# Kernel tuning notes

Measured on AMD Instinct MI355X. Metric: run time of the kernel, lower is better.

Reference implementation:

```python
import jax, jax.numpy as jnp
import numpy as np

N = 50000      # nodes
E = 500000     # edges
G = 8          # graphs in batch
H = 64         # latent width (message_passer out_channels)
FIN = 5        # raw node feature dim
MDIM = 3       # mask dim (last col = BC flag)
EF = 3         # edge feature dim
OUT = 4        # output dim
REPEATS = 4    # message passing repeats


def _mlp(h, w1, b1, w2, b2):
    return jnp.dot(jax.nn.relu(jnp.dot(h, w1) + b1), w2) + b2


def _seg_mean(v, idx, n):
    s = jax.ops.segment_sum(v, idx, num_segments=n)
    c = jax.ops.segment_sum(jnp.ones((v.shape[0], 1), v.dtype), idx, num_segments=n)
    return s / jnp.maximum(c, 1.0)


def _lin(k, fi, fo):
    return (jax.random.normal(k, (fi, fo), jnp.float32) / np.sqrt(fi),
            jnp.zeros((fo,), jnp.float32))


def setup_inputs() -> dict:
    key = jax.random.key(0)
    ks = jax.random.split(key, 16)
    x = jax.random.normal(ks[0], (N, FIN), jnp.float32)
    x_mask = jax.random.uniform(ks[1], (N, MDIM), jnp.float32)
    x_mask = x_mask.at[:, -1].set((x_mask[:, -1] > 0.9).astype(jnp.float32))
    edge_index = jax.random.randint(ks[2], (2, E), 0, N, jnp.int32)
    edge_attr = jax.random.normal(ks[3], (E, EF), jnp.float32)
    pos = jax.random.uniform(ks[4], (N, 2), jnp.float32)
    batch = jnp.sort(jax.random.randint(ks[5], (N,), 0, G, jnp.int32))
    enc_w1, enc_b1 = _lin(ks[6], FIN + MDIM, H)
    enc_w2, enc_b2 = _lin(ks[7], H, H)
    msg_w1, msg_b1 = _lin(ks[8], 2 * H + EF, H)
    msg_w2, msg_b2 = _lin(ks[9], H, H)
    upd_w1, upd_b1 = _lin(ks[10], 4 * H, H)
    upd_w2, upd_b2 = _lin(ks[11], H, H)
    dec_w1, dec_b1 = _lin(ks[12], H, H)
    dec_w2, dec_b2 = _lin(ks[13], H, OUT)
    return dict(x=x, x_mask=x_mask, edge_index=edge_index, edge_attr=edge_attr,
                pos=pos, batch=batch,
                enc_w1=enc_w1, enc_b1=enc_b1, enc_w2=enc_w2, enc_b2=enc_b2,
                msg_w1=msg_w1, msg_b1=msg_b1, msg_w2=msg_w2, msg_b2=msg_b2,
                upd_w1=upd_w1, upd_b1=upd_b1, upd_w2=upd_w2, upd_b2=upd_b2,
                dec_w1=dec_w1, dec_b1=dec_b1, dec_w2=dec_w2, dec_b2=dec_b2)


def reference(x, x_mask, edge_index, edge_attr, pos, batch,
              enc_w1, enc_b1, enc_w2, enc_b2,
              msg_w1, msg_b1, msg_w2, msg_b2,
              upd_w1, upd_b1, upd_w2, upd_b2,
              dec_w1, dec_b1, dec_w2, dec_b2):
    # x = concat([x, x_mask]); BC_idxs = x_mask[:, -1]
    bc = x_mask[:, -1:]                                   # [N,1] 0/1 BC flag
    h = _mlp(jnp.concatenate([x, x_mask], axis=1), enc_w1, enc_b1, enc_w2, enc_b2)
    # x_BC = scatter-mean of encoded BC nodes per graph (mask-weighted segment mean)
    bc_sum = jax.ops.segment_sum(h * bc, batch, num_segments=G)
    bc_cnt = jax.ops.segment_sum(bc, batch, num_segments=G)
    x_BC = bc_sum / jnp.maximum(bc_cnt, 1.0)              # [G,H]
    x_graph = _seg_mean(h, batch, G)                      # global_mean_pool [G,H]
    src, dst = edge_index[0], edge_index[1]
    for _ in range(REPEATS):
        # message: MLP over [x_src, x_dst, edge_attr], scatter-mean to dst
        m = _mlp(jnp.concatenate([h[src], h[dst], edge_attr], axis=1),
                 msg_w1, msg_b1, msg_w2, msg_b2)          # [E,H]
        agg = _seg_mean(m, dst, N)                        # [N,H]
        # node update conditioned on global and BC context, residual
        h = h + _mlp(jnp.concatenate([h, agg, x_graph[batch], x_BC[batch]], axis=1),
                     upd_w1, upd_b1, upd_w2, upd_b2)
        x_graph = _seg_mean(h, batch, G)                  # refreshed each repeat
    return _mlp(h, dec_w1, dec_b1, dec_w2, dec_b2)        # [N,OUT]
```

## Files before the change

kernel.cpp:

```cpp
#include <hip/hip_runtime.h>
#include <hip/hip_bf16.h>

#define NN 50000
#define EE 500000
#define GG 8
#define NB 196

#define SCALE_A 65536.0f
#define INV_SCALE_A (1.0f/65536.0f)
#define SCALE_G 16777216.0f
#define INV_SCALE_G (1.0f/16777216.0f)

using short8 = __attribute__((ext_vector_type(8))) short;
using f32x16 = __attribute__((ext_vector_type(16))) float;

__device__ __forceinline__ float4 ld4(const float* p){ return *reinterpret_cast<const float4*>(p); }

__device__ __forceinline__ short f2b(float f){
  union { __hip_bfloat16 b; short s; } u;
  u.b = __float2bfloat16(f);
  return u.s;
}

__global__ __launch_bounds__(256) void k_count(const int* __restrict__ dst, int* __restrict__ cnt){
  int e = blockIdx.x*256 + threadIdx.x;
  if (e < EE) atomicAdd(&cnt[dst[e]], 1);
}

__global__ __launch_bounds__(256) void k_scanA(const int* __restrict__ cnt, int* __restrict__ bsum){
  __shared__ int s[256];
  int t = threadIdx.x;
  int i = blockIdx.x*256 + t;
  s[t] = (i < NN) ? cnt[i] : 0;
  __syncthreads();
  for (int o=128;o>0;o>>=1){ if (t<o) s[t]+=s[t+o]; __syncthreads(); }
  if (t==0) bsum[blockIdx.x] = s[0];
}

__global__ __launch_bounds__(256) void k_scanB(const int* __restrict__ bsum, int* __restrict__ boff){
  __shared__ int s[256];
  int t = threadIdx.x;
  s[t] = (t < NB) ? bsum[t] : 0;
  __syncthreads();
  for (int o=1;o<256;o<<=1){
    int u = (t>=o) ? s[t-o] : 0;
    __syncthreads();
    s[t] += u;
    __syncthreads();
  }
  if (t < NB) boff[t] = (t==0) ? 0 : s[t-1];
}

__global__ __launch_bounds__(256) void k_scanC_prep(const int* __restrict__ cnt, const int* __restrict__ boff,
                                               int* __restrict__ offs,
                                               float* __restrict__ inv, const int* __restrict__ batch,
                                               const float* __restrict__ xm,
                                               float* __restrict__ ncnt, float* __restrict__ bccnt){
  __shared__ int s[256];
  __shared__ float lc[GG], lb[GG];
  int t = threadIdx.x;
  int i = blockIdx.x*256 + t;
  if (t < GG){ lc[t]=0.f; lb[t]=0.f; }
  int v = (i < NN) ? cnt[i] : 0;
  s[t] = v;
  __syncthreads();
  for (int o=1;o<256;o<<=1){
    int u = (t>=o) ? s[t-o] : 0;
    __syncthreads();
    s[t] += u;
    __syncthreads();
  }
  if (i < NN){
    offs[i] = boff[blockIdx.x] + s[t] - v;
    inv[i] = 1.0f / fmaxf((float)v, 1.0f);
    int g = batch[i];
    atomicAdd(&lc[g], 1.0f);
    atomicAdd(&lb[g], xm[i*3+2]);
  }
  __syncthreads();
  if (t < GG){ atomicAdd(&ncnt[t], lc[t]); atomicAdd(&bccnt[t], lb[t]); }
}

__global__ __launch_bounds__(256) void k_prep(const int* __restrict__ cnt, float* __restrict__ inv,
                       const int* __restrict__ batch, const float* __restrict__ xm,
                       float* __restrict__ ncnt, float* __restrict__ bccnt){
  __shared__ float lc[GG], lb[GG];
  int t = threadIdx.x;
  if (t < GG){ lc[t]=0.f; lb[t]=0.f; }
  __syncthreads();
  int i = blockIdx.x*256 + t;
  if (i < NN){
    inv[i] = 1.0f / fmaxf((float)cnt[i], 1.0f);
    int g = batch[i];
    atomicAdd(&lc[g], 1.0f);
    atomicAdd(&lb[g], xm[i*3+2]);
  }
  __syncthreads();
  if (t < GG){ atomicAdd(&ncnt[t], lc[t]); atomicAdd(&bccnt[t], lb[t]); }
}

__global__ __launch_bounds__(256) void k_scat1(const int* __restrict__ dst, int* __restrict__ offs,
                                               int* __restrict__ perm){
  int e = blockIdx.x*256 + threadIdx.x;
  if (e >= EE) return;
  int d = dst[e];
  int pos = atomicAdd(&offs[d], 1);
  perm[pos] = e;
}

__global__ __launch_bounds__(256) void k_scat2(const int* __restrict__ perm,
                                               const int* __restrict__ src, const int* __restrict__ dst,
                                               const float* __restrict__ ea,
                                               int* __restrict__ srcs_s, int* __restrict__ dsts_s,
                                               short* __restrict__ ea16){
  int i = blockIdx.x*256 + threadIdx.x;
  if (i >= EE) return;
  int e = perm[i];
  srcs_s[i] = src[e];
  dsts_s[i] = dst[e];
  int lo = ((int)(unsigned short)f2b(ea[(size_t)e*3+0])) |
           (((int)(unsigned short)f2b(ea[(size_t)e*3+1])) << 16);
  int hi = ((int)(unsigned short)f2b(ea[(size_t)e*3+2]));
  int2 v; v.x = lo; v.y = hi;
  *(int2*)(ea16 + (size_t)i*4) = v;
}

__device__ __forceinline__ void packone(const float* __restrict__ w, int Kreal, int idx, short* __restrict__ out){
  int k = idx >> 6, n = idx & 63;
  float v = (k < Kreal) ? w[k*64 + n] : 0.f;
  int ks = k >> 4, kl = k & 15;
  int lane = (n & 31) + 32*(kl >> 3);
  int e = kl & 7;
  out[(ks*2 + (n>>5))*512 + lane*8 + e] = f2b(v);
}

__global__ __launch_bounds__(256) void k_wpack(
    const float* __restrict__ mw1, const float* __restrict__ mw2,
    const float* __restrict__ uw1, const float* __restrict__ uw2,
    short* __restrict__ mw1p, short* __restrict__ mw2p,
    short* __restrict__ uw1p, short* __restrict__ uw2p){
  int gid = blockIdx.x*256 + threadIdx.x;
  int stride = gridDim.x*256;
  for (int i=gid; i<144*64; i+=stride) packone(mw1, 131, i, mw1p);
  for (int i=gid; i<64*64;  i+=stride) packone(mw2, 64,  i, mw2p);
  for (int i=gid; i<256*64; i+=stride) packone(uw1, 256, i, uw1p);
  for (int i=gid; i<64*64;  i+=stride) packone(uw2, 64,  i, uw2p);
}

__global__ __launch_bounds__(256) void k_enc(
    const float* __restrict__ x, const float* __restrict__ xm,
    const float* __restrict__ w1, const float* __restrict__ b1,
    const float* __restrict__ w2, const float* __restrict__ b2,
    float* __restrict__ h, short* __restrict__ h16){
  __shared__ float w1s[8*64];
  __shared__ float w2s[64*64];
  __shared__ float b1s[64], b2s[64];
  __shared__ float ols[4][64][17];
  int t = threadIdx.x;
  for (int i=t;i<8*64;i+=256) w1s[i]=w1[i];
  for (int i=t;i<64*64;i+=256) w2s[i]=w2[i];
  if (t<64){ b1s[t]=b1[t]; b2s[t]=b2[t]; }
  __syncthreads();
  const int w = t >> 6, lane = t & 63;
  const int base_w = blockIdx.x*256 + w*64;
  const int n = base_w + lane;
  const int nc = (n < NN) ? n : (NN-1);
  float in[8];
  #pragma unroll
  for (int k=0;k<5;k++) in[k] = x[nc*5+k];
  #pragma unroll
  for (int k=0;k<3;k++) in[5+k] = xm[nc*3+k];
  float hid[64];
  #pragma unroll
  for (int o=0;o<64;o++){
    float a = b1s[o];
    #pragma unroll
    for (int k=0;k<8;k++) a += in[k]*w1s[k*64+o];
    hid[o] = fmaxf(a, 0.f);
  }
  for (int c=0;c<4;c++){
    float a[16];
    #pragma unroll
    for (int j=0;j<16;j++) a[j] = b2s[c*16+j];
    for (int k=0;k<64;k++){
      float hv = hid[k];
      #pragma unroll
      for (int j=0;j<16;j++) a[j] += hv * w2s[k*64 + c*16 + j];
    }
    #pragma unroll
    for (int j=0;j<16;j++) ols[w][lane][j] = a[j];
    __syncthreads();
    #pragma unroll
    for (int p=0;p<4;p++){
      int nd = p*16 + (lane>>2);
      int jj = lane & 3;
      int ng = base_w + nd;
      if (ng < NN){
        float4 v = make_float4(ols[w][nd][jj*4+0], ols[w][nd][jj*4+1],
                               ols[w][nd][jj*4+2], ols[w][nd][jj*4+3]);
        *(float4*)(h + (size_t)ng*64 + c*16 + jj*4) = v;
      }
    }
    #pragma unroll
    for (int p=0;p<2;p++){
      int nd = p*32 + (lane>>1);
      int jj = (lane & 1)*8;
      int ng = base_w + nd;
      if (ng < NN){
        short8 s;
        #pragma unroll
        for (int q=0;q<8;q++) s[q] = f2b(ols[w][nd][jj+q]);
        *(short8*)(h16 + (size_t)ng*64 + c*16 + jj) = s;
      }
    }
    __syncthreads();
  }
}

__global__ __launch_bounds__(256) void k_gred(
    const float* __restrict__ h, const int* __restrict__ batch,
    const float* __restrict__ xm,
    unsigned long long* __restrict__ xg_sum, unsigned long long* __restrict__ xbc_sum, int withBC){
  __shared__ float ls[4][GG][64];
  __shared__ float lb[4][GG][64];
  int t = threadIdx.x;
  int d = t & 63, grp = t >> 6;
  for (int g=0; g<GG; g++){ ls[grp][g][d]=0.f; lb[grp][g][d]=0.f; }
  __syncthreads();
  for (int i = blockIdx.x*4 + grp; i < NN; i += gridDim.x*4){
    int g = batch[i];
    float v = h[(size_t)i*64 + d];
    ls[grp][g][d] += v;
    if (withBC) lb[grp][g][d] += v * xm[i*3+2];
  }
  __syncthreads();
  if (t < 64){
    for (int g=0; g<GG; g++){
      float s = ls[0][g][d]+ls[1][g][d]+ls[2][g][d]+ls[3][g][d];
      atomicAdd(&xg_sum[g*64+d], (unsigned long long)(long long)llrintf(s*SCALE_G));
    }
  } else if (withBC && t < 128){
    int dd = t & 63;
    for (int g=0; g<GG; g++){
      float s = lb[0][g][dd]+lb[1][g][dd]+lb[2][g][dd]+lb[3][g][dd];
      atomicAdd(&xbc_sum[g*64+dd], (unsigned long long)(long long)llrintf(s*SCALE_G));
    }
  }
}

__global__ void k_gfin(unsigned long long* __restrict__ xg_sum, const unsigned long long* __restrict__ xbc_sum,
                       const float* __restrict__ ncnt, const float* __restrict__ bccnt,
                       short* __restrict__ xg16, short* __restrict__ xbc16, int withBC){
  int t = threadIdx.x;
  int g = t >> 6;
  float sg = (float)(long long)xg_sum[t] * INV_SCALE_G;
  xg16[t] = f2b(sg / fmaxf(ncnt[g], 1.f));
  xg_sum[t] = 0;
  if (withBC){
    float sb = (float)(long long)xbc_sum[t] * INV_SCALE_G;
    xbc16[t] = f2b(sb / fmaxf(bccnt[g], 1.f));
  }
}

__global__ __launch_bounds__(64) void k_msg_s(
    const short* __restrict__ h16,
    const int* __restrict__ srcs_s, const int* __restrict__ dsts_s,
    const short* __restrict__ ea16,
    const short* __restrict__ w1p, const float* __restrict__ b1,
    const short* __restrict__ w2p, const float* __restrict__ b2,
    int* __restrict__ agg,
    unsigned long long* __restrict__ xg_sum, const unsigned long long* __restrict__ xbc_sum,
    const float* __restrict__ ncnt, const float* __restrict__ bccnt,
    short* __restrict__ xg16, short* __restrict__ xbc16, int withBC){
  __shared__ int buf[2304];
  const int t = threadIdx.x;
  if (blockIdx.x == 0){
    for (int i=t; i<GG*64; i+=64){
      int g = i >> 6;
      float sg = (float)(long long)xg_sum[i] * INV_SCALE_G;
      xg16[i] = f2b(sg / fmaxf(ncnt[g], 1.f));
      xg_sum[i] = 0;
      if (withBC){
        float sb = (float)(long long)xbc_sum[i] * INV_SCALE_G;
        xbc16[i] = f2b(sb / fmaxf(bccnt[g], 1.f));
      }
    }
  }
  const int nwg = gridDim.x;
  const int q = nwg >> 3, rm = nwg & 7;
  const int xcd = blockIdx.x & 7, idx = blockIdx.x >> 3;
  const int wg = (xcd < rm ? xcd*(q+1) : rm*(q+1) + (xcd-rm)*q) + idx;
  const int base = wg * 64;

  const int lane = t;
  const int r = lane & 31, khalf = lane >> 5;
  const int slot = base + lane;
  const int dl = (slot < EE) ? dsts_s[slot] : -1;

  const int eA = base + r, eB = base + 32 + r;
  const bool vA = eA < EE, vB = eB < EE;
  const int sA = vA ? srcs_s[eA] : 0;
  const int sB = vB ? srcs_s[eB] : 0;
  int dA = __shfl(dl, r);        if (dA < 0) dA = 0;
  int dB = __shfl(dl, 32 + r);   if (dB < 0) dB = 0;

  float b1v0 = b1[r], b1v1 = b1[32 + r];
  f32x16 acc00, acc01, acc10, acc11;
  #pragma unroll
  for (int j=0;j<16;j++){ acc00[j]=b1v0; acc01[j]=b1v1; acc10[j]=b1v0; acc11[j]=b1v1; }

  const short8* w1f = (const short8*)w1p;
  #pragma unroll
  for (int ks=0; ks<9; ks++){
    short8 a0, a1;
    if (ks < 8){
      long offA, offB;
      if (ks < 4){
        offA = (long)sA*64 + ks*16 + khalf*8;
        offB = (long)sB*64 + ks*16 + khalf*8;
      } else {
        offA = (long)dA*64 + (ks-4)*16 + khalf*8;
        offB = (long)dB*64 + (ks-4)*16 + khalf*8;
      }
      a0 = *(const short8*)(h16 + offA);
      a1 = *(const short8*)(h16 + offB);
    } else {
      #pragma unroll
      for (int j=0;j<8;j++){ a0[j]=0; a1[j]=0; }
      if (khalf == 0){
        if (vA){
          int2 v = *(const int2*)(ea16 + (size_t)eA*4);
          a0[0]=(short)v.x; a0[1]=(short)(v.x>>16); a0[2]=(short)v.y; a0[3]=(short)(v.y>>16);
        }
        if (vB){
          int2 v = *(const int2*)(ea16 + (size_t)eB*4);
          a1[0]=(short)v.x; a1[1]=(short)(v.x>>16); a1[2]=(short)v.y; a1[3]=(short)(v.y>>16);
        }
      }
    }
    short8 bf0 = w1f[(ks*2+0)*64 + lane];
    short8 bf1 = w1f[(ks*2+1)*64 + lane];
    acc00 = __builtin_amdgcn_mfma_f32_32x32x16_bf16(a0, bf0, acc00, 0, 0, 0);
    acc01 = __builtin_amdgcn_mfma_f32_32x32x16_bf16(a0, bf1, acc01, 0, 0, 0);
    acc10 = __builtin_amdgcn_mfma_f32_32x32x16_bf16(a1, bf0, acc10, 0, 0, 0);
    acc11 = __builtin_amdgcn_mfma_f32_32x32x16_bf16(a1, bf1, acc11, 0, 0, 0);
  }

  short* hw = (short*)&buf[0];
  #pragma unroll
  for (int reg=0; reg<16; reg++){
    int row = (reg&3) + 8*(reg>>2) + 4*khalf;
    hw[(row     )*72 + r     ] = f2b(fmaxf(acc00[reg], 0.f));
    hw[(row     )*72 + 32 + r] = f2b(fmaxf(acc01[reg], 0.f));
    hw[(row + 32)*72 + r     ] = f2b(fmaxf(acc10[reg], 0.f));
    hw[(row + 32)*72 + 32 + r] = f2b(fmaxf(acc11[reg], 0.f));
  }

  float b2v0 = b2[r], b2v1 = b2[32 + r];
  f32x16 c00, c01, c10, c11;
  #pragma unroll
  for (int j=0;j<16;j++){ c00[j]=b2v0; c01[j]=b2v1; c10[j]=b2v0; c11[j]=b2v1; }

  const short8* w2f = (const short8*)w2p;
  #pragma unroll
  for (int ks=0; ks<4; ks++){
    short8 p0 = *(const short8*)(hw + (r     )*72 + ks*16 + khalf*8);
    short8 p1 = *(const short8*)(hw + (32 + r)*72 + ks*16 + khalf*8);
    short8 bf0 = w2f[(ks*2+0)*64 + lane];
    short8 bf1 = w2f[(ks*2+1)*64 + lane];
    c00 = __builtin_amdgcn_mfma_f32_32x32x16_bf16(p0, bf0, c00, 0, 0, 0);
    c01 = __builtin_amdgcn_mfma_f32_32x32x16_bf16(p0, bf1, c01, 0, 0, 0);
    c10 = __builtin_amdgcn_mfma_f32_32x32x16_bf16(p1, bf0, c10, 0, 0, 0);
    c11 = __builtin_amdgcn_mfma_f32_32x32x16_bf16(p1, bf1, c11, 0, 0, 0);
  }

  int* mb = &buf[0];

  #pragma unroll
  for (int reg=0; reg<16; reg++){
    int row = (reg&3) + 8*(reg>>2) + 4*khalf;
    mb[row*65 + r     ] = __float2int_rn(c00[reg]*SCALE_A);
    mb[row*65 + 32 + r] = __float2int_rn(c01[reg]*SCALE_A);
  }
  {
    int run = 0;
    #pragma unroll
    for (int rr=0; rr<32; rr++){ run += mb[rr*65 + lane]; mb[rr*65 + lane] = run; }
    int cur = 0;
    while (cur < 32){
      int d = __shfl(dl, cur);
      unsigned long long diff = __ballot(dl != d);
      unsigned low = (unsigned)diff;
      unsigned rest = low & (0xFFFFFFFEu << cur);
      int end = rest ? (__ffs(rest) - 1) : 32;
      if (d >= 0){
        int s = mb[(end-1)*65 + lane] - (cur ? mb[(cur-1)*65 + lane] : 0);
        atomicAdd(&agg[(size_t)d*64 + lane], s);
      }
      cur = end;
    }
  }

  #pragma unroll
  for (int reg=0; reg<16; reg++){
    int row = (reg&3) + 8*(reg>>2) + 4*khalf;
    mb[row*65 + r     ] = __float2int_rn(c10[reg]*SCALE_A);
    mb[row*65 + 32 + r] = __float2int_rn(c11[reg]*SCALE_A);
  }
  {
    int run = 0;
    #pragma unroll
    for (int rr=0; rr<32; rr++){ run += mb[rr*65 + lane]; mb[rr*65 + lane] = run; }
    int cur = 0;
    while (cur < 32){
      int d = __shfl(dl, 32 + cur);
      unsigned long long diff = __ballot(dl != d);
      unsigned hi = (unsigned)(diff >> 32);
      unsigned rest = hi & (0xFFFFFFFEu << cur);
      int end = rest ? (__ffs(rest) - 1) : 32;
      if (d >= 0){
        int s = mb[(end-1)*65 + lane] - (cur ? mb[(cur-1)*65 + lane] : 0);
        atomicAdd(&agg[(size_t)d*64 + lane], s);
      }
      cur = end;
    }
  }
}

__global__ __launch_bounds__(256) void k_msg_atomic(
    const short* __restrict__ h16, const int* __restrict__ src, const int* __restrict__ dst,
    const float* __restrict__ ea,
    const short* __restrict__ w1p, const float* __restrict__ b1,
    const short* __restrict__ w2p, const float* __restrict__ b2,
    int* __restrict__ agg){
  __shared__ short hidT[4][64*72];
  const int t = threadIdx.x;
  const int w = t >> 6, lane = t & 63;
  const int r = lane & 31, khalf = lane >> 5;
  const int base = blockIdx.x*256 + w*64;
  const int eA = base + r, eB = base + 32 + r;
  const bool vA = eA < EE, vB = eB < EE;
  const int sA = vA ? src[eA] : 0, dA_ = vA ? dst[eA] : 0;
  const int sB = vB ? src[eB] : 0, dB_ = vB ? dst[eB] : 0;

  float b1v0 = b1[r], b1v1 = b1[32 + r];
  f32x16 acc00, acc01, acc10, acc11;
  #pragma unroll
  for (int j=0;j<16;j++){ acc00[j]=b1v0; acc01[j]=b1v1; acc10[j]=b1v0; acc11[j]=b1v1; }

  const short8* w1f = (const short8*)w1p;
  #pragma unroll
  for (int ks=0; ks<9; ks++){
    short8 a0, a1;
    if (ks < 8){
      long offA, offB;
      if (ks < 4){
        offA = (long)sA*64 + ks*16 + khalf*8;
        offB = (long)sB*64 + ks*16 + khalf*8;
      } else {
        offA = (long)dA_*64 + (ks-4)*16 + khalf*8;
        offB = (long)dB_*64 + (ks-4)*16 + khalf*8;
      }
      a0 = *(const short8*)(h16 + offA);
      a1 = *(const short8*)(h16 + offB);
    } else {
      #pragma unroll
      for (int j=0;j<8;j++){ a0[j]=0; a1[j]=0; }
      if (khalf == 0){
        if (vA){ a0[0]=f2b(ea[3*eA]); a0[1]=f2b(ea[3*eA+1]); a0[2]=f2b(ea[3*eA+2]); }
        if (vB){ a1[0]=f2b(ea[3*eB]); a1[1]=f2b(ea[3*eB+1]); a1[2]=f2b(ea[3*eB+2]); }
      }
    }
    short8 bf0 = w1f[(ks*2+0)*64 + lane];
    short8 bf1 = w1f[(ks*2+1)*64 + lane];
    acc00 = __builtin_amdgcn_mfma_f32_32x32x16_bf16(a0, bf0, acc00, 0, 0, 0);
    acc01 = __builtin_amdgcn_mfma_f32_32x32x16_bf16(a0, bf1, acc01, 0, 0, 0);
    acc10 = __builtin_amdgcn_mfma_f32_32x32x16_bf16(a1, bf0, acc10, 0, 0, 0);
    acc11 = __builtin_amdgcn_mfma_f32_32x32x16_bf16(a1, bf1, acc11, 0, 0, 0);
  }

  short* hw = &hidT[w][0];
  #pragma unroll
  for (int reg=0; reg<16; reg++){
    int row = (reg&3) + 8*(reg>>2) + 4*khalf;
    hw[(row     )*72 + r     ] = f2b(fmaxf(acc00[reg], 0.f));
    hw[(row     )*72 + 32 + r] = f2b(fmaxf(acc01[reg], 0.f));
    hw[(row + 32)*72 + r     ] = f2b(fmaxf(acc10[reg], 0.f));
    hw[(row + 32)*72 + 32 + r] = f2b(fmaxf(acc11[reg], 0.f));
  }

  float b2v0 = b2[r], b2v1 = b2[32 + r];
  f32x16 c00, c01, c10, c11;
  #pragma unroll
  for (int j=0;j<16;j++){ c00[j]=b2v0; c01[j]=b2v1; c10[j]=b2v0; c11[j]=b2v1; }

  const short8* w2f = (const short8*)w2p;
  #pragma unroll
  for (int ks=0; ks<4; ks++){
    short8 a0 = *(const short8*)(hw + (r     )*72 + ks*16 + khalf*8);
    short8 a1 = *(const short8*)(hw + (32 + r)*72 + ks*16 + khalf*8);
    short8 bf0 = w2f[(ks*2+0)*64 + lane];
    short8 bf1 = w2f[(ks*2+1)*64 + lane];
    c00 = __builtin_amdgcn_mfma_f32_32x32x16_bf16(a0, bf0, c00, 0, 0, 0);
    c01 = __builtin_amdgcn_mfma_f32_32x32x16_bf16(a0, bf1, c01, 0, 0, 0);
    c10 = __builtin_amdgcn_mfma_f32_32x32x16_bf16(a1, bf0, c10, 0, 0, 0);
    c11 = __builtin_amdgcn_mfma_f32_32x32x16_bf16(a1, bf1, c11, 0, 0, 0);
  }

  #pragma unroll
  for (int reg=0; reg<16; reg++){
    int row = (reg&3) + 8*(reg>>2) + 4*khalf;
    int e0r = base + row;
    int e1r = base + 32 + row;
    int d0 = __shfl(dA_, row);
    int d1 = __shfl(dB_, row);
    if (e0r < EE){
      atomicAdd(&agg[(size_t)d0*64 + r     ], __float2int_rn(c00[reg]*SCALE_A));
      atomicAdd(&agg[(size_t)d0*64 + 32 + r], __float2int_rn(c01[reg]*SCALE_A));
    }
    if (e1r < EE){
      atomicAdd(&agg[(size_t)d1*64 + r     ], __float2int_rn(c10[reg]*SCALE_A));
      atomicAdd(&agg[(size_t)d1*64 + 32 + r], __float2int_rn(c11[reg]*SCALE_A));
    }
  }
}

__global__ __launch_bounds__(64) void k_upd(
    float* __restrict__ h32, short* __restrict__ h16,
    int* __restrict__ agg, const float* __restrict__ inv,
    const int* __restrict__ batch,
    const short* __restrict__ xg16, const short* __restrict__ xbc16,
    const short* __restrict__ w1p, const float* __restrict__ b1,
    const short* __restrict__ w2p, const float* __restrict__ b2,
    unsigned long long* __restrict__ xg_sum, int withG){
  __shared__ short hidT[32*72];
  __shared__ unsigned long long gs[GG*64];
  const int t = threadIdx.x;
  for (int i=t; i<GG*64; i+=64) gs[i]=0;
  __syncthreads();

  const int lane = t;
  const int r = lane & 31, khalf = lane >> 5;
  const int n0 = blockIdx.x*32;
  const int n = n0 + r;
  const int nc = (n < NN) ? n : (NN-1);
  const int g = batch[nc];
  const float sc = inv[nc] * INV_SCALE_A;

  float b1v0 = b1[r], b1v1 = b1[32 + r];
  f32x16 a0acc, a1acc;
  #pragma unroll
  for (int j=0;j<16;j++){ a0acc[j]=b1v0; a1acc[j]=b1v1; }

  const short8* w1f = (const short8*)w1p;
  #pragma unroll
  for (int ks=0; ks<16; ks++){
    short8 a;
    int so = (ks & 3)*16 + khalf*8;
    if (ks < 4){
      a = *(const short8*)(h16 + (long)nc*64 + so);
    } else if (ks < 8){
      int4 i0 = *(const int4*)(agg + (long)nc*64 + so);
      int4 i1 = *(const int4*)(agg + (long)nc*64 + so + 4);
      if (n < NN){
        *(int4*)(agg + (long)nc*64 + so)     = make_int4(0,0,0,0);
        *(int4*)(agg + (long)nc*64 + so + 4) = make_int4(0,0,0,0);
      }
      a[0]=f2b((float)i0.x*sc); a[1]=f2b((float)i0.y*sc); a[2]=f2b((float)i0.z*sc); a[3]=f2b((float)i0.w*sc);
      a[4]=f2b((float)i1.x*sc); a[5]=f2b((float)i1.y*sc); a[6]=f2b((float)i1.z*sc); a[7]=f2b((float)i1.w*sc);
    } else if (ks < 12){
      a = *(const short8*)(xg16 + g*64 + so);
    } else {
      a = *(const short8*)(xbc16 + g*64 + so);
    }
    short8 bf0 = w1f[(ks*2+0)*64 + lane];
    short8 bf1 = w1f[(ks*2+1)*64 + lane];
    a0acc = __builtin_amdgcn_mfma_f32_32x32x16_bf16(a, bf0, a0acc, 0, 0, 0);
    a1acc = __builtin_amdgcn_mfma_f32_32x32x16_bf16(a, bf1, a1acc, 0, 0, 0);
  }

  short* hw = hidT;
  #pragma unroll
  for (int reg=0; reg<16; reg++){
    int row = (reg&3) + 8*(reg>>2) + 4*khalf;
    hw[row*72 + r     ] = f2b(fmaxf(a0acc[reg], 0.f));
    hw[row*72 + 32 + r] = f2b(fmaxf(a1acc[reg], 0.f));
  }

  float b2v0 = b2[r], b2v1 = b2[32 + r];
  f32x16 c0, c1;
  #pragma unroll
  for (int j=0;j<16;j++){ c0[j]=b2v0; c1[j]=b2v1; }

  const short8* w2f = (const short8*)w2p;
  #pragma unroll
  for (int ks=0; ks<4; ks++){
    short8 a = *(const short8*)(hw + r*72 + ks*16 + khalf*8);
    short8 bf0 = w2f[(ks*2+0)*64 + lane];
    short8 bf1 = w2f[(ks*2+1)*64 + lane];
    c0 = __builtin_amdgcn_mfma_f32_32x32x16_bf16(a, bf0, c0, 0, 0, 0);
    c1 = __builtin_amdgcn_mfma_f32_32x32x16_bf16(a, bf1, c1, 0, 0, 0);
  }

  const bool doG = (withG != 0);
  const int g0 = __shfl(g, 0), g31 = __shfl(g, 31);
  const bool uni = (g0 == g31);
  long long s0 = 0, s1 = 0;
  #pragma unroll
  for (int reg=0; reg<16; reg++){
    int row = (reg&3) + 8*(reg>>2) + 4*khalf;
    int gg = __shfl(g, row);
    int nn = n0 + row;
    if (nn < NN){
      size_t i0 = (size_t)nn*64 + r;
      float v0 = h32[i0] + c0[reg];
      float v1 = h32[i0+32] + c1[reg];
      h32[i0] = v0;    h16[i0] = f2b(v0);
      h32[i0+32] = v1; h16[i0+32] = f2b(v1);
      if (doG){
        long long q0 = llrintf(v0*SCALE_G), q1 = llrintf(v1*SCALE_G);
        if (uni){ s0 += q0; s1 += q1; }
        else {
          atomicAdd(&gs[gg*64 + r     ], (unsigned long long)q0);
          atomicAdd(&gs[gg*64 + 32 + r], (unsigned long long)q1);
        }
      }
    }
  }
  if (doG && uni && (s0|s1)){
    atomicAdd(&gs[g0*64 + r     ], (unsigned long long)s0);
    atomicAdd(&gs[g0*64 + 32 + r], (unsigned long long)s1);
  }
  __syncthreads();
  if (doG){
    for (int i=t; i<GG*64; i+=64){
      unsigned long long v = gs[i];
      if (v) atomicAdd(&xg_sum[i], v);
    }
  }
}

__global__ __launch_bounds__(256) void k_dec(
    const float* __restrict__ h,
    const float* __restrict__ w1, const float* __restrict__ b1,
    const float* __restrict__ w2, const float* __restrict__ b2,
    float* __restrict__ out){
  __shared__ float w1s[64*64];
  __shared__ float w2s[64*4];
  __shared__ float b1s[64], b2s[4];
  int t=threadIdx.x;
  for (int i=t;i<64*64;i+=256) w1s[i]=w1[i];
  for (int i=t;i<256;i+=256) w2s[i]=w2[i];
  if (t<64) b1s[t]=b1[t];
  if (t<4) b2s[t]=b2[t];
  __syncthreads();
  int n = blockIdx.x*256+t;
  if (n>=NN) return;
  float xr[64];
  #pragma unroll
  for (int k=0;k<16;k++){
    float4 v = ld4(h + (size_t)n*64 + k*4);
    xr[k*4+0]=v.x; xr[k*4+1]=v.y; xr[k*4+2]=v.z; xr[k*4+3]=v.w;
  }
  float a0=b2s[0],a1=b2s[1],a2=b2s[2],a3=b2s[3];
  for (int o=0;o<64;o++){
    float a=b1s[o];
    #pragma unroll
    for (int k=0;k<64;k++) a += xr[k]*w1s[k*64+o];
    a = fmaxf(a,0.f);
    a0 += a*w2s[o*4+0]; a1 += a*w2s[o*4+1]; a2 += a*w2s[o*4+2]; a3 += a*w2s[o*4+3];
  }
  out[(size_t)n*4+0]=a0; out[(size_t)n*4+1]=a1; out[(size_t)n*4+2]=a2; out[(size_t)n*4+3]=a3;
}

extern "C" void kernel_launch(void* const* d_in, const int* in_sizes, int n_in,
                              void* d_out, int out_size, void* d_ws, size_t ws_size,
                              hipStream_t stream){
  const float* x   = (const float*)d_in[0];
  const float* xm  = (const float*)d_in[1];
  const int*   ei  = (const int*)d_in[2];
  const float* ea  = (const float*)d_in[3];
  const int* batch = (const int*)d_in[5];
  const float* enc_w1=(const float*)d_in[6],  *enc_b1=(const float*)d_in[7];
  const float* enc_w2=(const float*)d_in[8],  *enc_b2=(const float*)d_in[9];
  const float* msg_w1=(const float*)d_in[10], *msg_b1=(const float*)d_in[11];
  const float* msg_w2=(const float*)d_in[12], *msg_b2=(const float*)d_in[13];
  const float* upd_w1=(const float*)d_in[14], *upd_b1=(const float*)d_in[15];
  const float* upd_w2=(const float*)d_in[16], *upd_b2=(const float*)d_in[17];
  const float* dec_w1=(const float*)d_in[18], *dec_b1=(const float*)d_in[19];
  const float* dec_w2=(const float*)d_in[20], *dec_b2=(const float*)d_in[21];
  const int* srcp = ei;
  const int* dstp = ei + EE;

  char* ws = (char*)d_ws;
  float* h32     = (float*)(ws + 0);
  int*   agg     = (int*)  (ws + 12800000);
  int*   cnt     = (int*)  (ws + 25600000);
  unsigned long long* xg_sum  = (unsigned long long*)(ws + 25800000);
  unsigned long long* xbc_sum = (unsigned long long*)(ws + 25804096);
  float* ncnt    = (float*)(ws + 25808192);
  float* bccnt   = (float*)(ws + 25808224);
  short* h16     = (short*)(ws + 25808256);
  float* inv     = (float*)(ws + 32208256);
  short* xg16    = (short*)(ws + 32408256);
  short* xbc16   = (short*)(ws + 32409280);
  short* mw1p    = (short*)(ws + 32410304);
  short* mw2p    = (short*)(ws + 32428736);
  short* uw1p    = (short*)(ws + 32436928);
  short* uw2p    = (short*)(ws + 32469696);
  int*   offs    = (int*)  (ws + 32477888);
  int*   srcs_s  = (int*)  (ws + 32677888);
  int*   dsts_s  = (int*)  (ws + 34678784);
  short* ea16s   = (short*)(ws + 36679680);
  int*   bsum    = (int*)  (ws + 40681472);
  int*   boff    = (int*)  (ws + 40682272);
  int*   perm    = (int*)  (ws + 40683072);
  const size_t WS_NEED_SORT = 42683968;
  const int useSort = (ws_size >= WS_NEED_SORT) ? 1 : 0;

  hipMemsetAsync(ws + 12800000, 0, 13008256, stream);
  k_wpack<<<34, 256, 0, stream>>>(msg_w1, msg_w2, upd_w1, upd_w2, mw1p, mw2p, uw1p, uw2p);
  k_count<<<(EE+255)/256, 256, 0, stream>>>(dstp, cnt);
  if (useSort){
    k_scanA<<<NB, 256, 0, stream>>>(cnt, bsum);
    k_scanB<<<1, 256, 0, stream>>>(bsum, boff);
    k_scanC_prep<<<NB, 256, 0, stream>>>(cnt, boff, offs, inv, batch, xm, ncnt, bccnt);
    k_scat1<<<(EE+255)/256, 256, 0, stream>>>(dstp, offs, perm);
    k_scat2<<<(EE+255)/256, 256, 0, stream>>>(perm, srcp, dstp, ea, srcs_s, dsts_s, ea16s);
  } else {
    k_prep<<<(NN+255)/256, 256, 0, stream>>>(cnt, inv, batch, xm, ncnt, bccnt);
  }
  k_enc<<<(NN+255)/256, 256, 0, stream>>>(x, xm, enc_w1, enc_b1, enc_w2, enc_b2, h32, h16);
  k_gred<<<512, 256, 0, stream>>>(h32, batch, xm, xg_sum, xbc_sum, 1);

  if (useSort){
    for (int rp=0; rp<4; rp++){
      k_msg_s<<<(EE+63)/64, 64, 0, stream>>>(h16, srcs_s, dsts_s, ea16s, mw1p, msg_b1, mw2p, msg_b2, agg,
                                             xg_sum, xbc_sum, ncnt, bccnt, xg16, xbc16, (rp==0)?1:0);
      int withG = (rp < 3) ? 1 : 0;
      k_upd<<<(NN+31)/32, 64, 0, stream>>>(h32, h16, agg, inv, batch, xg16, xbc16, uw1p, upd_b1, uw2p, upd_b2, xg_sum, withG);
    }
  } else {
    k_gfin<<<1, 512, 0, stream>>>(xg_sum, xbc_sum, ncnt, bccnt, xg16, xbc16, 1);
    for (int rp=0; rp<4; rp++){
      k_msg_atomic<<<(EE+255)/256, 256, 0, stream>>>(h16, srcp, dstp, ea, mw1p, msg_b1, mw2p, msg_b2, agg);
      int withG = (rp < 3) ? 1 : 0;
      k_upd<<<(NN+31)/32, 64, 0, stream>>>(h32, h16, agg, inv, batch, xg16, xbc16, uw1p, upd_b1, uw2p, upd_b2, xg_sum, withG);
      if (withG) k_gfin<<<1, 512, 0, stream>>>(xg_sum, xbc_sum, ncnt, bccnt, xg16, xbc16, 0);
    }
  }
  k_dec<<<(NN+255)/256, 256, 0, stream>>>(h32, dec_w1, dec_b1, dec_w2, dec_b2, (float*)d_out);
}
```

Before: 399.8 us.

## Fuse message pass and node update into per-node-block round kernel

Replaces the separate edge-parallel message kernel and node update kernel with one kernel per round. Each workgroup owns 32 destination nodes, walks their dst-sorted edge range, accumulates messages in LDS instead of global atomics, and then runs the update MLP in the same workgroup. h16 is double-buffered so neighbour reads in a round see the previous h, and graph-mean sums go to per-round buffers. This removes the agg round trip through global memory, the global atomics and the memset, at the cost of load imbalance from uneven node degrees and a grid that is about ten times smaller.

```diff
diff --git a/kernel.cpp b/kernel.cpp
--- a/kernel.cpp
+++ b/kernel.cpp
@@ -262,167 +262,256 @@
   }
 }
 
-__global__ __launch_bounds__(64) void k_msg_s(
-    const short* __restrict__ h16,
+__global__ __launch_bounds__(64) void k_round(
+    const short* __restrict__ h16in, short* __restrict__ h16out,
+    float* __restrict__ h32,
     const int* __restrict__ srcs_s, const int* __restrict__ dsts_s,
     const short* __restrict__ ea16,
-    const short* __restrict__ w1p, const float* __restrict__ b1,
-    const short* __restrict__ w2p, const float* __restrict__ b2,
-    int* __restrict__ agg,
-    unsigned long long* __restrict__ xg_sum, const unsigned long long* __restrict__ xbc_sum,
+    const int* __restrict__ offsEnd, const int* __restrict__ cnt,
+    const float* __restrict__ inv, const int* __restrict__ batch,
+    const unsigned long long* __restrict__ xgs_prev,
+    unsigned long long* __restrict__ xgs_next,
+    const unsigned long long* __restrict__ xbc_sum,
     const float* __restrict__ ncnt, const float* __restrict__ bccnt,
-    short* __restrict__ xg16, short* __restrict__ xbc16, int withBC){
+    const short* __restrict__ mw1p, const float* __restrict__ mb1,
+    const short* __restrict__ mw2p, const float* __restrict__ mb2,
+    const short* __restrict__ uw1p, const float* __restrict__ ub1,
+    const short* __restrict__ uw2p, const float* __restrict__ ub2,
+    int withG){
+  __shared__ int nodeagg[32*65];
   __shared__ int buf[2304];
+  __shared__ short xgloc[GG*64];
+  __shared__ short xbcloc[GG*64];
   const int t = threadIdx.x;
-  if (blockIdx.x == 0){
-    for (int i=t; i<GG*64; i+=64){
-      int g = i >> 6;
-      float sg = (float)(long long)xg_sum[i] * INV_SCALE_G;
-      xg16[i] = f2b(sg / fmaxf(ncnt[g], 1.f));
-      xg_sum[i] = 0;
-      if (withBC){
-        float sb = (float)(long long)xbc_sum[i] * INV_SCALE_G;
-        xbc16[i] = f2b(sb / fmaxf(bccnt[g], 1.f));
-      }
-    }
-  }
-  const int nwg = gridDim.x;
-  const int q = nwg >> 3, rm = nwg & 7;
-  const int xcd = blockIdx.x & 7, idx = blockIdx.x >> 3;
-  const int wg = (xcd < rm ? xcd*(q+1) : rm*(q+1) + (xcd-rm)*q) + idx;
-  const int base = wg * 64;
-
-  const int lane = t;
-  const int r = lane & 31, khalf = lane >> 5;
-  const int slot = base + lane;
-  const int dl = (slot < EE) ? dsts_s[slot] : -1;
-
-  const int eA = base + r, eB = base + 32 + r;
-  const bool vA = eA < EE, vB = eB < EE;
-  const int sA = vA ? srcs_s[eA] : 0;
-  const int sB = vB ? srcs_s[eB] : 0;
-  int dA = __shfl(dl, r);        if (dA < 0) dA = 0;
-  int dB = __shfl(dl, 32 + r);   if (dB < 0) dB = 0;
-
-  float b1v0 = b1[r], b1v1 = b1[32 + r];
-  f32x16 acc00, acc01, acc10, acc11;
-  #pragma unroll
-  for (int j=0;j<16;j++){ acc00[j]=b1v0; acc01[j]=b1v1; acc10[j]=b1v0; acc11[j]=b1v1; }
-
-  const short8* w1f = (const short8*)w1p;
-  #pragma unroll
-  for (int ks=0; ks<9; ks++){
-    short8 a0, a1;
-    if (ks < 8){
-      long offA, offB;
-      if (ks < 4){
-        offA = (long)sA*64 + ks*16 + khalf*8;
-        offB = (long)sB*64 + ks*16 + khalf*8;
+  const int lane = t, r = lane & 31, khalf = lane >> 5;
+
+  for (int i=t; i<GG*64; i+=64){
+    int g = i >> 6;
+    xgloc[i]  = f2b((float)(long long)xgs_prev[i] * INV_SCALE_G / fmaxf(ncnt[g], 1.f));
+    xbcloc[i] = f2b((float)(long long)xbc_sum[i] * INV_SCALE_G / fmaxf(bccnt[g], 1.f));
+  }
+  for (int i=t; i<32*65; i+=64) nodeagg[i] = 0;
+
+  const int n0 = blockIdx.x * 32;
+  const int nLast = ((n0 + 32 <= NN) ? (n0 + 32) : NN) - 1;
+  const int eStart = offsEnd[n0] - cnt[n0];
+  const int eEnd   = offsEnd[nLast];
+
+  const float b1v0 = mb1[r], b1v1 = mb1[32 + r];
+  const float b2v0 = mb2[r], b2v1 = mb2[32 + r];
+  const short8* w1f = (const short8*)mw1p;
+  const short8* w2f = (const short8*)mw2p;
+  short* hw = (short*)&buf[0];
+  int* mb = &buf[0];
+
+  for (int ebase = eStart; ebase < eEnd; ebase += 64){
+    const int slot = ebase + lane;
+    const int dl = (slot < eEnd) ? (dsts_s[slot] - n0) : -1;
+    const int slotA = ebase + r, slotB = ebase + 32 + r;
+    const bool vA = slotA < eEnd, vB = slotB < eEnd;
+    const int sA = vA ? srcs_s[slotA] : 0;
+    const int sB = vB ? srcs_s[slotB] : 0;
+    int dAl = __shfl(dl, r);      const int dA = n0 + (dAl < 0 ? 0 : dAl);
+    int dBl = __shfl(dl, 32 + r); const int dB = n0 + (dBl < 0 ? 0 : dBl);
+
+    f32x16 acc00, acc01, acc10, acc11;
+    #pragma unroll
+    for (int j=0;j<16;j++){ acc00[j]=b1v0; acc01[j]=b1v1; acc10[j]=b1v0; acc11[j]=b1v1; }
+
+    #pragma unroll
+    for (int ks=0; ks<9; ks++){
+      short8 a0, a1;
+      if (ks < 8){
+        long offA = (ks < 4) ? ((long)sA*64 + ks*16 + khalf*8) : ((long)dA*64 + (ks-4)*16 + khalf*8);
+        long offB = (ks < 4) ? ((long)sB*64 + ks*16 + khalf*8) : ((long)dB*64 + (ks-4)*16 + khalf*8);
+        a0 = *(const short8*)(h16in + offA);
+        a1 = *(const short8*)(h16in + offB);
       } else {
-        offA = (long)dA*64 + (ks-4)*16 + khalf*8;
-        offB = (long)dB*64 + (ks-4)*16 + khalf*8;
-      }
-      a0 = *(const short8*)(h16 + offA);
-      a1 = *(const short8*)(h16 + offB);
+        #pragma unroll
+        for (int j=0;j<8;j++){ a0[j]=0; a1[j]=0; }
+        if (khalf == 0){
+          if (vA){
+            int2 v = *(const int2*)(ea16 + (size_t)slotA*4);
+            a0[0]=(short)v.x; a0[1]=(short)(v.x>>16); a0[2]=(short)v.y; a0[3]=(short)(v.y>>16);
+          }
+          if (vB){
+            int2 v = *(const int2*)(ea16 + (size_t)slotB*4);
+            a1[0]=(short)v.x; a1[1]=(short)(v.x>>16); a1[2]=(short)v.y; a1[3]=(short)(v.y>>16);
+          }
+        }
+      }
+      short8 bf0 = w1f[(ks*2+0)*64 + lane];
+      short8 bf1 = w1f[(ks*2+1)*64 + lane];
+      acc00 = __builtin_amdgcn_mfma_f32_32x32x16_bf16(a0, bf0, acc00, 0, 0, 0);
+      acc01 = __builtin_amdgcn_mfma_f32_32x32x16_bf16(a0, bf1, acc01, 0, 0, 0);
+      acc10 = __builtin_amdgcn_mfma_f32_32x32x16_bf16(a1, bf0, acc10, 0, 0, 0);
+      acc11 = __builtin_amdgcn_mfma_f32_32x32x16_bf16(a1, bf1, acc11, 0, 0, 0);
+    }
+
+    #pragma unroll
+    for (int reg=0; reg<16; reg++){
+      int row = (reg&3) + 8*(reg>>2) + 4*khalf;
+      hw[(row     )*72 + r     ] = f2b(fmaxf(acc00[reg], 0.f));
+      hw[(row     )*72 + 32 + r] = f2b(fmaxf(acc01[reg], 0.f));
+      hw[(row + 32)*72 + r     ] = f2b(fmaxf(acc10[reg], 0.f));
+      hw[(row + 32)*72 + 32 + r] = f2b(fmaxf(acc11[reg], 0.f));
+    }
+
+    f32x16 c00, c01, c10, c11;
+    #pragma unroll
+    for (int j=0;j<16;j++){ c00[j]=b2v0; c01[j]=b2v1; c10[j]=b2v0; c11[j]=b2v1; }
+
+    #pragma unroll
+    for (int ks=0; ks<4; ks++){
+      short8 p0 = *(const short8*)(hw + (r     )*72 + ks*16 + khalf*8);
+      short8 p1 = *(const short8*)(hw + (32 + r)*72 + ks*16 + khalf*8);
+      short8 bf0 = w2f[(ks*2+0)*64 + lane];
+      short8 bf1 = w2f[(ks*2+1)*64 + lane];
+      c00 = __builtin_amdgcn_mfma_f32_32x32x16_bf16(p0, bf0, c00, 0, 0, 0);
+      c01 = __builtin_amdgcn_mfma_f32_32x32x16_bf16(p0, bf1, c01, 0, 0, 0);
+      c10 = __builtin_amdgcn_mfma_f32_32x32x16_bf16(p1, bf0, c10, 0, 0, 0);
+      c11 = __builtin_amdgcn_mfma_f32_32x32x16_bf16(p1, bf1, c11, 0, 0, 0);
+    }
+
+    #pragma unroll
+    for (int reg=0; reg<16; reg++){
+      int row = (reg&3) + 8*(reg>>2) + 4*khalf;
+      mb[row*65 + r     ] = __float2int_rn(c00[reg]*SCALE_A);
+      mb[row*65 + 32 + r] = __float2int_rn(c01[reg]*SCALE_A);
+    }
+    {
+      int run = 0;
+      #pragma unroll
+      for (int rr=0; rr<32; rr++){ run += mb[rr*65 + lane]; mb[rr*65 + lane] = run; }
+      int cur = 0;
+      while (cur < 32){
+        int d = __shfl(dl, cur);
+        unsigned long long diff = __ballot(dl != d);
+        unsigned low = (unsigned)diff;
+        unsigned rest = low & (0xFFFFFFFEu << cur);
+        int end = rest ? (__ffs(rest) - 1) : 32;
+        if (d >= 0){
+          int s = mb[(end-1)*65 + lane] - (cur ? mb[(cur-1)*65 + lane] : 0);
+          nodeagg[d*65 + lane] += s;
+        }
+        cur = end;
+      }
+    }
+
+    #pragma unroll
+    for (int reg=0; reg<16; reg++){
+      int row = (reg&3) + 8*(reg>>2) + 4*khalf;
+      mb[row*65 + r     ] = __float2int_rn(c10[reg]*SCALE_A);
+      mb[row*65 + 32 + r] = __float2int_rn(c11[reg]*SCALE_A);
+    }
+    {
+      int run = 0;
+      #pragma unroll
+      for (int rr=0; rr<32; rr++){ run += mb[rr*65 + lane]; mb[rr*65 + lane] = run; }
+      int cur = 0;
+      while (cur < 32){
+        int d = __shfl(dl, 32 + cur);
+        unsigned long long diff = __ballot(dl != d);
+        unsigned hi = (unsigned)(diff >> 32);
+        unsigned rest = hi & (0xFFFFFFFEu << cur);
+        int end = rest ? (__ffs(rest) - 1) : 32;
+        if (d >= 0){
+          int s = mb[(end-1)*65 + lane] - (cur ? mb[(cur-1)*65 + lane] : 0);
+          nodeagg[d*65 + lane] += s;
+        }
+        cur = end;
+      }
+    }
+  }
+
+  const int n = n0 + r;
+  const int nc = (n < NN) ? n : (NN-1);
+  const int g = batch[nc];
+  const float sc = inv[nc] * INV_SCALE_A;
+
+  float ub1v0 = ub1[r], ub1v1 = ub1[32 + r];
+  f32x16 a0acc, a1acc;
+  #pragma unroll
+  for (int j=0;j<16;j++){ a0acc[j]=ub1v0; a1acc[j]=ub1v1; }
+
+  const short8* u1f = (const short8*)uw1p;
+  #pragma unroll
+  for (int ks=0; ks<16; ks++){
+    short8 a;
+    int so = (ks & 3)*16 + khalf*8;
+    if (ks < 4){
+      a = *(const short8*)(h16in + (long)nc*64 + so);
+    } else if (ks < 8){
+      #pragma unroll
+      for (int j=0;j<8;j++) a[j] = f2b((float)nodeagg[r*65 + so + j] * sc);
+    } else if (ks < 12){
+      a = *(const short8*)(xgloc + g*64 + so);
     } else {
-      #pragma unroll
-      for (int j=0;j<8;j++){ a0[j]=0; a1[j]=0; }
-      if (khalf == 0){
-        if (vA){
-          int2 v = *(const int2*)(ea16 + (size_t)eA*4);
-          a0[0]=(short)v.x; a0[1]=(short)(v.x>>16); a0[2]=(short)v.y; a0[3]=(short)(v.y>>16);
-        }
-        if (vB){
-          int2 v = *(const int2*)(ea16 + (size_t)eB*4);
-          a1[0]=(short)v.x; a1[1]=(short)(v.x>>16); a1[2]=(short)v.y; a1[3]=(short)(v.y>>16);
-        }
-      }
-    }
-    short8 bf0 = w1f[(ks*2+0)*64 + lane];
-    short8 bf1 = w1f[(ks*2+1)*64 + lane];
-    acc00 = __builtin_amdgcn_mfma_f32_32x32x16_bf16(a0, bf0, acc00, 0, 0, 0);
-    acc01 = __builtin_amdgcn_mfma_f32_32x32x16_bf16(a0, bf1, acc01, 0, 0, 0);
-    acc10 = __builtin_amdgcn_mfma_f32_32x32x16_bf16(a1, bf0, acc10, 0, 0, 0);
-    acc11 = __builtin_amdgcn_mfma_f32_32x32x16_bf16(a1, bf1, acc11, 0, 0, 0);
-  }
-
-  short* hw = (short*)&buf[0];
+      a = *(const short8*)(xbcloc + g*64 + so);
+    }
+    short8 bf0 = u1f[(ks*2+0)*64 + lane];
+    short8 bf1 = u1f[(ks*2+1)*64 + lane];
+    a0acc = __builtin_amdgcn_mfma_f32_32x32x16_bf16(a, bf0, a0acc, 0, 0, 0);
+    a1acc = __builtin_amdgcn_mfma_f32_32x32x16_bf16(a, bf1, a1acc, 0, 0, 0);
+  }
+
   #pragma unroll
   for (int reg=0; reg<16; reg++){
     int row = (reg&3) + 8*(reg>>2) + 4*khalf;
-    hw[(row     )*72 + r     ] = f2b(fmaxf(acc00[reg], 0.f));
-    hw[(row     )*72 + 32 + r] = f2b(fmaxf(acc01[reg], 0.f));
-    hw[(row + 32)*72 + r     ] = f2b(fmaxf(acc10[reg], 0.f));
-    hw[(row + 32)*72 + 32 + r] = f2b(fmaxf(acc11[reg], 0.f));
-  }
-
-  float b2v0 = b2[r], b2v1 = b2[32 + r];
-  f32x16 c00, c01, c10, c11;
-  #pragma unroll
-  for (int j=0;j<16;j++){ c00[j]=b2v0; c01[j]=b2v1; c10[j]=b2v0; c11[j]=b2v1; }
-
-  const short8* w2f = (const short8*)w2p;
+    hw[row*72 + r     ] = f2b(fmaxf(a0acc[reg], 0.f));
+    hw[row*72 + 32 + r] = f2b(fmaxf(a1acc[reg], 0.f));
+  }
+
+  float ub2v0 = ub2[r], ub2v1 = ub2[32 + r];
+  f32x16 c0, c1;
+  #pragma unroll
+  for (int j=0;j<16;j++){ c0[j]=ub2v0; c1[j]=ub2v1; }
+
+  const short8* u2f = (const short8*)uw2p;
   #pragma unroll
   for (int ks=0; ks<4; ks++){
-    short8 p0 = *(const short8*)(hw + (r     )*72 + ks*16 + khalf*8);
-    short8 p1 = *(const short8*)(hw + (32 + r)*72 + ks*16 + khalf*8);
-    short8 bf0 = w2f[(ks*2+0)*64 + lane];
-    short8 bf1 = w2f[(ks*2+1)*64 + lane];
-    c00 = __builtin_amdgcn_mfma_f32_32x32x16_bf16(p0, bf0, c00, 0, 0, 0);
-    c01 = __builtin_amdgcn_mfma_f32_32x32x16_bf16(p0, bf1, c01, 0, 0, 0);
-    c10 = __builtin_amdgcn_mfma_f32_32x32x16_bf16(p1, bf0, c10, 0, 0, 0);
-    c11 = __builtin_amdgcn_mfma_f32_32x32x16_bf16(p1, bf1, c11, 0, 0, 0);
-  }
-
-  int* mb = &buf[0];
-
+    short8 a = *(const short8*)(hw + r*72 + ks*16 + khalf*8);
+    short8 bf0 = u2f[(ks*2+0)*64 + lane];
+    short8 bf1 = u2f[(ks*2+1)*64 + lane];
+    c0 = __builtin_amdgcn_mfma_f32_32x32x16_bf16(a, bf0, c0, 0, 0, 0);
+    c1 = __builtin_amdgcn_mfma_f32_32x32x16_bf16(a, bf1, c1, 0, 0, 0);
+  }
+
+  unsigned long long* gs = (unsigned long long*)&nodeagg[0];
+  const bool doG = (withG != 0);
+  if (doG){ for (int i=t; i<GG*64; i+=64) gs[i] = 0; }
+  const int g0 = __shfl(g, 0), g31 = __shfl(g, 31);
+  const bool uni = (g0 == g31);
+  long long s0 = 0, s1 = 0;
   #pragma unroll
   for (int reg=0; reg<16; reg++){
     int row = (reg&3) + 8*(reg>>2) + 4*khalf;
-    mb[row*65 + r     ] = __float2int_rn(c00[reg]*SCALE_A);
-    mb[row*65 + 32 + r] = __float2int_rn(c01[reg]*SCALE_A);
-  }
-  {
-    int run = 0;
-    #pragma unroll
-    for (int rr=0; rr<32; rr++){ run += mb[rr*65 + lane]; mb[rr*65 + lane] = run; }
-    int cur = 0;
-    while (cur < 32){
-      int d = __shfl(dl, cur);
-      unsigned long long diff = __ballot(dl != d);
-      unsigned low = (unsigned)diff;
-      unsigned rest = low & (0xFFFFFFFEu << cur);
-      int end = rest ? (__ffs(rest) - 1) : 32;
-      if (d >= 0){
-        int s = mb[(end-1)*65 + lane] - (cur ? mb[(cur-1)*65 + lane] : 0);
-        atomicAdd(&agg[(size_t)d*64 + lane], s);
-      }
-      cur = end;
-    }
-  }
-
-  #pragma unroll
-  for (int reg=0; reg<16; reg++){
-    int row = (reg&3) + 8*(reg>>2) + 4*khalf;
-    mb[row*65 + r     ] = __float2int_rn(c10[reg]*SCALE_A);
-    mb[row*65 + 32 + r] = __float2int_rn(c11[reg]*SCALE_A);
-  }
-  {
-    int run = 0;
-    #pragma unroll
-    for (int rr=0; rr<32; rr++){ run += mb[rr*65 + lane]; mb[rr*65 + lane] = run; }
-    int cur = 0;
-    while (cur < 32){
-      int d = __shfl(dl, 32 + cur);
-      unsigned long long diff = __ballot(dl != d);
-      unsigned hi = (unsigned)(diff >> 32);
-      unsigned rest = hi & (0xFFFFFFFEu << cur);
-      int end = rest ? (__ffs(rest) - 1) : 32;
-      if (d >= 0){
-        int s = mb[(end-1)*65 + lane] - (cur ? mb[(cur-1)*65 + lane] : 0);
-        atomicAdd(&agg[(size_t)d*64 + lane], s);
-      }
-      cur = end;
+    int gg = __shfl(g, row);
+    int nn = n0 + row;
+    if (nn < NN){
+      size_t i0 = (size_t)nn*64 + r;
+      float v0 = h32[i0] + c0[reg];
+      float v1 = h32[i0+32] + c1[reg];
+      h32[i0] = v0;    h16out[i0] = f2b(v0);
+      h32[i0+32] = v1; h16out[i0+32] = f2b(v1);
+      if (doG){
+        long long q0 = llrintf(v0*SCALE_G), q1 = llrintf(v1*SCALE_G);
+        if (uni){ s0 += q0; s1 += q1; }
+        else {
+          atomicAdd(&gs[gg*64 + r     ], (unsigned long long)q0);
+          atomicAdd(&gs[gg*64 + 32 + r], (unsigned long long)q1);
+        }
+      }
+    }
+  }
+  if (doG && uni && (s0|s1)){
+    atomicAdd(&gs[g0*64 + r     ], (unsigned long long)s0);
+    atomicAdd(&gs[g0*64 + 32 + r], (unsigned long long)s1);
+  }
+  if (doG){
+    for (int i=t; i<GG*64; i+=64){
+      unsigned long long v = gs[i];
+      if (v) atomicAdd(&xgs_next[i], v);
     }
   }
 }
@@ -696,29 +785,31 @@
   float* h32     = (float*)(ws + 0);
   int*   agg     = (int*)  (ws + 12800000);
   int*   cnt     = (int*)  (ws + 25600000);
-  unsigned long long* xg_sum  = (unsigned long long*)(ws + 25800000);
-  unsigned long long* xbc_sum = (unsigned long long*)(ws + 25804096);
-  float* ncnt    = (float*)(ws + 25808192);
-  float* bccnt   = (float*)(ws + 25808224);
-  short* h16     = (short*)(ws + 25808256);
-  float* inv     = (float*)(ws + 32208256);
-  short* xg16    = (short*)(ws + 32408256);
-  short* xbc16   = (short*)(ws + 32409280);
-  short* mw1p    = (short*)(ws + 32410304);
-  short* mw2p    = (short*)(ws + 32428736);
-  short* uw1p    = (short*)(ws + 32436928);
-  short* uw2p    = (short*)(ws + 32469696);
-  int*   offs    = (int*)  (ws + 32477888);
-  int*   srcs_s  = (int*)  (ws + 32677888);
-  int*   dsts_s  = (int*)  (ws + 34678784);
-  short* ea16s   = (short*)(ws + 36679680);
-  int*   bsum    = (int*)  (ws + 40681472);
-  int*   boff    = (int*)  (ws + 40682272);
-  int*   perm    = (int*)  (ws + 40683072);
-  const size_t WS_NEED_SORT = 42683968;
+  unsigned long long* xgs = (unsigned long long*)(ws + 25800000);
+  unsigned long long* xbc_sum = (unsigned long long*)(ws + 25816384);
+  float* ncnt    = (float*)(ws + 25820480);
+  float* bccnt   = (float*)(ws + 25820512);
+  short* h16a    = (short*)(ws + 25820544);
+  float* inv     = (float*)(ws + 32220544);
+  short* xg16    = (short*)(ws + 32420544);
+  short* xbc16   = (short*)(ws + 32421568);
+  short* mw1p    = (short*)(ws + 32422592);
+  short* mw2p    = (short*)(ws + 32441024);
+  short* uw1p    = (short*)(ws + 32449216);
+  short* uw2p    = (short*)(ws + 32481984);
+  int*   offs    = (int*)  (ws + 32490176);
+  int*   srcs_s  = (int*)  (ws + 32690176);
+  int*   dsts_s  = (int*)  (ws + 34691072);
+  short* ea16s   = (short*)(ws + 36691968);
+  int*   bsum    = (int*)  (ws + 40693760);
+  int*   boff    = (int*)  (ws + 40694560);
+  int*   perm    = (int*)  (ws + 40695360);
+  const size_t WS_NEED_SORT = 42696256;
   const int useSort = (ws_size >= WS_NEED_SORT) ? 1 : 0;
-
-  hipMemsetAsync(ws + 12800000, 0, 13008256, stream);
+  short* h16b    = (short*)agg;
+
+  hipMemsetAsync(ws + 25600000, 0, 220544, stream);
+  if (!useSort) hipMemsetAsync(agg, 0, 12800000, stream);
   k_wpack<<<34, 256, 0, stream>>>(msg_w1, msg_w2, upd_w1, upd_w2, mw1p, mw2p, uw1p, uw2p);
   k_count<<<(EE+255)/256, 256, 0, stream>>>(dstp, cnt);
   if (useSort){
@@ -730,23 +821,26 @@
   } else {
     k_prep<<<(NN+255)/256, 256, 0, stream>>>(cnt, inv, batch, xm, ncnt, bccnt);
   }
-  k_enc<<<(NN+255)/256, 256, 0, stream>>>(x, xm, enc_w1, enc_b1, enc_w2, enc_b2, h32, h16);
-  k_gred<<<512, 256, 0, stream>>>(h32, batch, xm, xg_sum, xbc_sum, 1);
+  k_enc<<<(NN+255)/256, 256, 0, stream>>>(x, xm, enc_w1, enc_b1, enc_w2, enc_b2, h32, h16a);
+  k_gred<<<512, 256, 0, stream>>>(h32, batch, xm, &xgs[0], xbc_sum, 1);
 
   if (useSort){
     for (int rp=0; rp<4; rp++){
-      k_msg_s<<<(EE+63)/64, 64, 0, stream>>>(h16, srcs_s, dsts_s, ea16s, mw1p, msg_b1, mw2p, msg_b2, agg,
-                                             xg_sum, xbc_sum, ncnt, bccnt, xg16, xbc16, (rp==0)?1:0);
+      const short* hin  = (rp & 1) ? h16b : h16a;
+      short*       hout = (rp & 1) ? h16a : h16b;
       int withG = (rp < 3) ? 1 : 0;
-      k_upd<<<(NN+31)/32, 64, 0, stream>>>(h32, h16, agg, inv, batch, xg16, xbc16, uw1p, upd_b1, uw2p, upd_b2, xg_sum, withG);
+      k_round<<<(NN+31)/32, 64, 0, stream>>>(
+          hin, hout, h32, srcs_s, dsts_s, ea16s, offs, cnt, inv, batch,
+          &xgs[(size_t)rp*512], &xgs[(size_t)(rp+1 < 4 ? rp+1 : 3)*512], xbc_sum, ncnt, bccnt,
+          mw1p, msg_b1, mw2p, msg_b2, uw1p, upd_b1, uw2p, upd_b2, withG);
     }
   } else {
-    k_gfin<<<1, 512, 0, stream>>>(xg_sum, xbc_sum, ncnt, bccnt, xg16, xbc16, 1);
+    k_gfin<<<1, 512, 0, stream>>>(&xgs[0], xbc_sum, ncnt, bccnt, xg16, xbc16, 1);
     for (int rp=0; rp<4; rp++){
-      k_msg_atomic<<<(EE+255)/256, 256, 0, stream>>>(h16, srcp, dstp, ea, mw1p, msg_b1, mw2p, msg_b2, agg);
+      k_msg_atomic<<<(EE+255)/256, 256, 0, stream>>>(h16a, srcp, dstp, ea, mw1p, msg_b1, mw2p, msg_b2, agg);
       int withG = (rp < 3) ? 1 : 0;
-      k_upd<<<(NN+31)/32, 64, 0, stream>>>(h32, h16, agg, inv, batch, xg16, xbc16, uw1p, upd_b1, uw2p, upd_b2, xg_sum, withG);
-      if (withG) k_gfin<<<1, 512, 0, stream>>>(xg_sum, xbc_sum, ncnt, bccnt, xg16, xbc16, 0);
+      k_upd<<<(NN+31)/32, 64, 0, stream>>>(h32, h16a, agg, inv, batch, xg16, xbc16, uw1p, upd_b1, uw2p, upd_b2, &xgs[0], withG);
+      if (withG) k_gfin<<<1, 512, 0, stream>>>(&xgs[0], xbc_sum, ncnt, bccnt, xg16, xbc16, 0);
     }
   }
   k_dec<<<(NN+255)/256, 256, 0, stream>>>(h32, dec_w1, dec_b1, dec_w2, dec_b2, (float*)d_out);
```

New measurement: 601.4 us. 1.5x slower.
